# Kernel optimization log

Measured on AMD Instinct MI355X. Metric: run time of the kernel, lower is better.

The kernel has to match this reference:

```python
import jax, jax.numpy as jnp
import numpy as np

# PointPillars KITTI config (matches init_kwargs)
VX, VY = 0.16, 0.16
PC_RANGE = (0.0, -39.68, -3.0, 69.12, 39.68, 1.0)
X_OFFSET = VX / 2 + PC_RANGE[0]          # 0.08
Y_OFFSET = VY / 2 + PC_RANGE[1]          # -39.60
Z_CONST = (PC_RANGE[5] + PC_RANGE[2]) / 2  # -1.0
GRID_X = int((PC_RANGE[3] - PC_RANGE[0]) / VX)  # 432
GRID_Y = int((PC_RANGE[4] - PC_RANGE[1]) / VY)  # 496
BN_EPS = 1e-3


def setup_inputs() -> dict:
    key = jax.random.key(0)
    ks = jax.random.split(key, 6)
    B, PPB, N, C = 4, 12000, 32, 64
    P = B * PPB
    # raw pillar point features (x,y,z,intensity)
    pillars = jax.random.normal(ks[0], (P, N, 4), dtype=jnp.float32)
    # unique pillar cells per batch element (real voxelization never duplicates cells)
    cells = jax.vmap(lambda k: jax.random.permutation(k, GRID_X * GRID_Y)[:PPB])(
        jax.random.split(ks[1], B))  # [B, PPB]
    coors_x = (cells // GRID_Y).reshape(-1).astype(jnp.int64)
    coors_y = (cells % GRID_Y).reshape(-1).astype(jnp.int64)
    coors_b = jnp.repeat(jnp.arange(B, dtype=jnp.int64), PPB)
    npoints = jax.random.randint(ks[2], (P,), 1, N + 1, dtype=jnp.int32)
    W = jax.random.normal(ks[3], (C, 10), dtype=jnp.float32) * 0.1
    gamma = jnp.ones((C,), dtype=jnp.float32)
    beta = jnp.zeros((C,), dtype=jnp.float32)
    return {"pillars": pillars, "W": W, "gamma": gamma, "beta": beta,
            "coors_x": coors_x, "coors_y": coors_y, "coors_b": coors_b,
            "npoints": npoints, "batch_size": B}


def reference(pillars, W, gamma, beta, coors_x, coors_y, coors_b, npoints, batch_size):
    dt = pillars.dtype
    P, N, _ = pillars.shape
    npf = npoints.astype(dt)
    # offset from pillar point-centroid (sum includes zero padding, as in torch)
    mean_xyz = jnp.sum(pillars[:, :, :3], axis=1, keepdims=True) / npf[:, None, None]
    off_center = pillars[:, :, :3] - mean_xyz  # [P,N,3]
    # offset from pillar cell center
    xo = pillars[:, :, 0:1] - (coors_x.astype(dt)[:, None, None] * VX + X_OFFSET)
    yo = pillars[:, :, 1:2] - (coors_y.astype(dt)[:, None, None] * VY + Y_OFFSET)
    zo = jnp.full_like(xo, Z_CONST)
    # features after the in-place overwrite of channels 0,1:
    # [x_off, y_off, z, intensity, dx, dy, dz, x_off, y_off, z_const]
    feats = jnp.concatenate(
        [xo, yo, pillars[:, :, 2:4], off_center, xo, yo, zo], axis=-1)  # [P,N,10]
    mask = (jnp.arange(N)[None, :] < npoints[:, None]).astype(dt)  # [P,N]
    feats = feats * mask[:, :, None]
    # per-point linear (no bias) -> BN (training-mode batch stats over P,N) -> ReLU
    x = jnp.einsum('pnf,cf->pnc', feats, W)  # [P,N,C]
    mu = jnp.mean(x, axis=(0, 1))
    var = jnp.var(x, axis=(0, 1))
    x = (x - mu) * jax.lax.rsqrt(var + BN_EPS) * gamma + beta
    x = jax.nn.relu(x)
    x_max = jnp.max(x, axis=1)  # [P,C] segment-max over points per pillar
    # scatter into dense BEV grid, then [B, C, Y, X]
    C = x_max.shape[-1]
    grid = jnp.zeros((batch_size, GRID_X, GRID_Y, C), dtype=dt)
    grid = grid.at[coors_b, coors_x, coors_y].set(x_max)
    return jnp.transpose(grid, (0, 3, 2, 1))
```

## Files before the change

### kernel.cpp

```cpp
#include <hip/hip_runtime.h>
#include <stdint.h>

#define GRID_X 432
#define GRID_Y 496
#define NB 4
#define NPTS 32
#define NC 64
#define NSLOTS 64
#define CELLS (GRID_Y * GRID_X)

constexpr float VXc = 0.16f, VYc = 0.16f;
constexpr float X_OFFSET = 0.08f, Y_OFFSET = -39.60f, Z_CONST = -1.0f;
constexpr float BN_EPS = 1e-3f;

__global__ __launch_bounds__(256) void pillar_stats_kernel(
    const float* __restrict__ pillars, const float* __restrict__ W,
    const int* __restrict__ cx, const int* __restrict__ cy,
    const int* __restrict__ cb, const int* __restrict__ npoints,
    float* __restrict__ vmax, float* __restrict__ vmin, int* __restrict__ map,
    double* __restrict__ dsum, double* __restrict__ dsq, int P)
{
    __shared__ float4 pts[4][NPTS];
    __shared__ float pinfo[4][4];
    __shared__ float ssum[4][NC], ssq[4][NC];

    const int tid = threadIdx.x;
    const int p0 = blockIdx.x * 4;

    if (tid < 128) {
        int pl = tid >> 5, n = tid & 31;
        int p = p0 + pl;
        float4 v = make_float4(0.f, 0.f, 0.f, 0.f);
        if (p < P) v = ((const float4*)pillars)[(size_t)p * NPTS + n];
        pts[pl][n] = v;
        float sx = v.x, sy = v.y, sz = v.z;
        #pragma unroll
        for (int m = 16; m >= 1; m >>= 1) {
            sx += __shfl_xor(sx, m, 32);
            sy += __shfl_xor(sy, m, 32);
            sz += __shfl_xor(sz, m, 32);
        }
        if (n == 0 && p < P) {
            float npf = (float)npoints[p];
            pinfo[pl][0] = sx / npf;
            pinfo[pl][1] = sy / npf;
            pinfo[pl][2] = sz / npf;
            pinfo[pl][3] = npf;
        }
    }
    if (tid >= 128 && tid < 132) {
        int p = p0 + (tid - 128);
        if (p < P) {
            int b = cb[p];
            map[(size_t)b * CELLS + (size_t)cy[p] * GRID_X + cx[p]] = p;
        }
    }
    __syncthreads();

    const int pl = tid >> 6, c = tid & 63;
    const int p = p0 + pl;
    float ssu = 0.f, sq2 = 0.f;
    if (p < P) {
        const float* w = W + c * 10;
        float w0 = w[0], w1 = w[1], w2 = w[2], w3 = w[3], w4 = w[4];
        float w5 = w[5], w6 = w[6], w7 = w[7], w8 = w[8], w9 = w[9];
        float Aw = w0 + w4 + w7;
        float Bw = w1 + w5 + w8;
        float Cw = w2 + w6;
        float Dw = w3;
        float cxo = cx[p] * VXc + X_OFFSET;
        float cyo = cy[p] * VYc + Y_OFFSET;
        float mx = pinfo[pl][0], my = pinfo[pl][1], mz = pinfo[pl][2];
        int np = (int)pinfo[pl][3];
        float E = -cxo * (w0 + w7) - cyo * (w1 + w8)
                  - mx * w4 - my * w5 - mz * w6 + Z_CONST * w9;
        float smax = -1e30f, smin = 1e30f;
        #pragma unroll
        for (int n = 0; n < NPTS; ++n) {
            float4 pt = pts[pl][n];
            float v = E;
            v = fmaf(pt.x, Aw, v);
            v = fmaf(pt.y, Bw, v);
            v = fmaf(pt.z, Cw, v);
            v = fmaf(pt.w, Dw, v);
            v = (n < np) ? v : 0.0f;
            smax = fmaxf(smax, v);
            smin = fminf(smin, v);
            ssu += v;
            sq2 = fmaf(v, v, sq2);
        }
        vmax[(size_t)p * NC + c] = smax;
        vmin[(size_t)p * NC + c] = smin;
    }
    ssum[pl][c] = ssu;
    ssq[pl][c]  = sq2;
    __syncthreads();
    if (tid < NC) {
        float s = ssum[0][tid] + ssum[1][tid] + ssum[2][tid] + ssum[3][tid];
        float q = ssq[0][tid]  + ssq[1][tid]  + ssq[2][tid]  + ssq[3][tid];
        int slot = blockIdx.x & (NSLOTS - 1);
        atomicAdd(&dsum[slot * NC + tid], (double)s);
        atomicAdd(&dsq[slot * NC + tid],  (double)q);
    }
}

__global__ void bn_params_kernel(const double* __restrict__ dsum,
                                 const double* __restrict__ dsq,
                                 const float* __restrict__ gamma,
                                 const float* __restrict__ beta,
                                 float* __restrict__ st, int P)
{
    int c = threadIdx.x;
    if (c < NC) {
        double s = 0.0, q = 0.0;
        for (int i = 0; i < NSLOTS; ++i) { s += dsum[i * NC + c]; q += dsq[i * NC + c]; }
        double cnt = (double)P * NPTS;
        double mu = s / cnt;
        double var = q / cnt - mu * mu;
        float scale = gamma[c] * (float)(1.0 / sqrt(var + (double)BN_EPS));
        float shift = beta[c] - (float)mu * scale;
        st[c] = scale;
        st[NC + c] = shift;
    }
}

__global__ __launch_bounds__(256) void scatter_out_kernel(
    const int* __restrict__ map, const float* __restrict__ vmax,
    const float* __restrict__ vmin, const float* __restrict__ st,
    float* __restrict__ out)
{
    const int q = blockIdx.x * 256 + threadIdx.x;
    const int b = blockIdx.y;
    const int m = map[(size_t)b * CELLS + q];
    float* ob = out + (size_t)b * NC * CELLS + q;
    #pragma unroll 8
    for (int c = 0; c < NC; ++c) {
        float r = 0.0f;
        if (m >= 0) {
            float s = st[c], t = st[NC + c];
            float v = (s >= 0.0f) ? vmax[(size_t)m * NC + c] : vmin[(size_t)m * NC + c];
            r = fmaxf(fmaf(s, v, t), 0.0f);
        }
        ob[(size_t)c * CELLS] = r;
    }
}

extern "C" void kernel_launch(void* const* d_in, const int* in_sizes, int n_in,
                              void* d_out, int out_size, void* d_ws, size_t ws_size,
                              hipStream_t stream) {
    const float* pillars = (const float*)d_in[0];
    const float* W       = (const float*)d_in[1];
    const float* gamma   = (const float*)d_in[2];
    const float* beta    = (const float*)d_in[3];
    const int*   cx      = (const int*)d_in[4];
    const int*   cy      = (const int*)d_in[5];
    const int*   cb      = (const int*)d_in[6];
    const int*   np      = (const int*)d_in[7];
    const int P = in_sizes[4];

    char* ws = (char*)d_ws;
    float* vmax = (float*)ws;
    float* vmin = vmax + (size_t)P * NC;
    int*   map  = (int*)(vmin + (size_t)P * NC);
    size_t mapN = (size_t)NB * CELLS;
    double* dsum = (double*)(((uintptr_t)(map + mapN) + 255) & ~(uintptr_t)255);
    double* dsq  = dsum + NSLOTS * NC;
    float*  st   = (float*)(dsq + NSLOTS * NC);

    hipMemsetAsync(map, 0xFF, mapN * sizeof(int), stream);
    hipMemsetAsync(dsum, 0, (size_t)NSLOTS * NC * 2 * sizeof(double), stream);

    pillar_stats_kernel<<<(P + 3) / 4, 256, 0, stream>>>(
        pillars, W, cx, cy, cb, np, vmax, vmin, map, dsum, dsq, P);
    bn_params_kernel<<<1, 64, 0, stream>>>(dsum, dsq, gamma, beta, st, P);
    scatter_out_kernel<<<dim3(CELLS / 256, NB), 256, 0, stream>>>(
        map, vmax, vmin, st, (float*)d_out);
}
```

Measured before the change: 287.2 us.

## Fold gamma sign into features to drop vmin; vectorize scatter with float4 stores

Each channel's projected values are multiplied by the sign of gamma, and scale now uses |gamma|. This makes a single max buffer enough for the BN-ReLU-max reduction, so the vmin array and its reads and writes go away. The scatter kernel now handles four grid cells per thread: it loads the map as int4, keeps scale and shift in shared memory, and writes float4 outputs. This is meant to cut store transactions on the large dense output. The cost is four gathered vsel reads per thread per channel.

```diff
diff --git a/kernel.cpp b/kernel.cpp
--- a/kernel.cpp
+++ b/kernel.cpp
@@ -8,6 +8,7 @@
 #define NC 64
 #define NSLOTS 64
 #define CELLS (GRID_Y * GRID_X)
+#define QUADS (CELLS / 4)
 
 constexpr float VXc = 0.16f, VYc = 0.16f;
 constexpr float X_OFFSET = 0.08f, Y_OFFSET = -39.60f, Z_CONST = -1.0f;
@@ -15,13 +16,14 @@
 
 __global__ __launch_bounds__(256) void pillar_stats_kernel(
     const float* __restrict__ pillars, const float* __restrict__ W,
+    const float* __restrict__ gamma,
     const int* __restrict__ cx, const int* __restrict__ cy,
     const int* __restrict__ cb, const int* __restrict__ npoints,
-    float* __restrict__ vmax, float* __restrict__ vmin, int* __restrict__ map,
+    float* __restrict__ vsel, int* __restrict__ map,
     double* __restrict__ dsum, double* __restrict__ dsq, int P)
 {
     __shared__ float4 pts[4][NPTS];
-    __shared__ float pinfo[4][4];
+    __shared__ float pinfo[4][6];
     __shared__ float ssum[4][NC], ssq[4][NC];
 
     const int tid = threadIdx.x;
@@ -46,6 +48,8 @@
             pinfo[pl][1] = sy / npf;
             pinfo[pl][2] = sz / npf;
             pinfo[pl][3] = npf;
+            pinfo[pl][4] = cx[p] * VXc + X_OFFSET;
+            pinfo[pl][5] = cy[p] * VYc + Y_OFFSET;
         }
     }
     if (tid >= 128 && tid < 132) {
@@ -64,17 +68,18 @@
         const float* w = W + c * 10;
         float w0 = w[0], w1 = w[1], w2 = w[2], w3 = w[3], w4 = w[4];
         float w5 = w[5], w6 = w[6], w7 = w[7], w8 = w[8], w9 = w[9];
-        float Aw = w0 + w4 + w7;
-        float Bw = w1 + w5 + w8;
-        float Cw = w2 + w6;
-        float Dw = w3;
-        float cxo = cx[p] * VXc + X_OFFSET;
-        float cyo = cy[p] * VYc + Y_OFFSET;
+        float sg = (gamma[c] >= 0.0f) ? 1.0f : -1.0f;
+        float Aw = sg * (w0 + w4 + w7);
+        float Bw = sg * (w1 + w5 + w8);
+        float Cw = sg * (w2 + w6);
+        float Dw = sg * w3;
+        float cxo = pinfo[pl][4];
+        float cyo = pinfo[pl][5];
         float mx = pinfo[pl][0], my = pinfo[pl][1], mz = pinfo[pl][2];
         int np = (int)pinfo[pl][3];
-        float E = -cxo * (w0 + w7) - cyo * (w1 + w8)
-                  - mx * w4 - my * w5 - mz * w6 + Z_CONST * w9;
-        float smax = -1e30f, smin = 1e30f;
+        float E = sg * (-cxo * (w0 + w7) - cyo * (w1 + w8)
+                        - mx * w4 - my * w5 - mz * w6 + Z_CONST * w9);
+        float smax = -1e30f;
         #pragma unroll
         for (int n = 0; n < NPTS; ++n) {
             float4 pt = pts[pl][n];
@@ -85,12 +90,10 @@
             v = fmaf(pt.w, Dw, v);
             v = (n < np) ? v : 0.0f;
             smax = fmaxf(smax, v);
-            smin = fminf(smin, v);
             ssu += v;
             sq2 = fmaf(v, v, sq2);
         }
-        vmax[(size_t)p * NC + c] = smax;
-        vmin[(size_t)p * NC + c] = smin;
+        vsel[(size_t)p * NC + c] = smax;
     }
     ssum[pl][c] = ssu;
     ssq[pl][c]  = sq2;
@@ -117,7 +120,7 @@
         double cnt = (double)P * NPTS;
         double mu = s / cnt;
         double var = q / cnt - mu * mu;
-        float scale = gamma[c] * (float)(1.0 / sqrt(var + (double)BN_EPS));
+        float scale = fabsf(gamma[c]) * (float)(1.0 / sqrt(var + (double)BN_EPS));
         float shift = beta[c] - (float)mu * scale;
         st[c] = scale;
         st[NC + c] = shift;
@@ -125,23 +128,34 @@
 }
 
 __global__ __launch_bounds__(256) void scatter_out_kernel(
-    const int* __restrict__ map, const float* __restrict__ vmax,
-    const float* __restrict__ vmin, const float* __restrict__ st,
-    float* __restrict__ out)
+    const int* __restrict__ map, const float* __restrict__ vsel,
+    const float* __restrict__ st, float* __restrict__ out)
 {
-    const int q = blockIdx.x * 256 + threadIdx.x;
+    __shared__ float ssc[NC], ssh[NC];
+    if (threadIdx.x < NC) {
+        ssc[threadIdx.x] = st[threadIdx.x];
+        ssh[threadIdx.x] = st[NC + threadIdx.x];
+    }
+    __syncthreads();
+    const int q4 = blockIdx.x * 256 + threadIdx.x;
     const int b = blockIdx.y;
-    const int m = map[(size_t)b * CELLS + q];
-    float* ob = out + (size_t)b * NC * CELLS + q;
+    if (q4 >= QUADS) return;
+    const int4 m4 = ((const int4*)(map + (size_t)b * CELLS))[q4];
+    const bool bx = m4.x >= 0, by = m4.y >= 0, bz = m4.z >= 0, bw = m4.w >= 0;
+    const float* vpx = vsel + (size_t)(bx ? m4.x : 0) * NC;
+    const float* vpy = vsel + (size_t)(by ? m4.y : 0) * NC;
+    const float* vpz = vsel + (size_t)(bz ? m4.z : 0) * NC;
+    const float* vpw = vsel + (size_t)(bw ? m4.w : 0) * NC;
+    float* ob = out + (size_t)b * NC * CELLS + (size_t)q4 * 4;
     #pragma unroll 8
     for (int c = 0; c < NC; ++c) {
-        float r = 0.0f;
-        if (m >= 0) {
-            float s = st[c], t = st[NC + c];
-            float v = (s >= 0.0f) ? vmax[(size_t)m * NC + c] : vmin[(size_t)m * NC + c];
-            r = fmaxf(fmaf(s, v, t), 0.0f);
-        }
-        ob[(size_t)c * CELLS] = r;
+        float sc = ssc[c], sh = ssh[c];
+        float4 r;
+        r.x = bx ? fmaxf(fmaf(sc, vpx[c], sh), 0.0f) : 0.0f;
+        r.y = by ? fmaxf(fmaf(sc, vpy[c], sh), 0.0f) : 0.0f;
+        r.z = bz ? fmaxf(fmaf(sc, vpz[c], sh), 0.0f) : 0.0f;
+        r.w = bw ? fmaxf(fmaf(sc, vpw[c], sh), 0.0f) : 0.0f;
+        *(float4*)(ob + (size_t)c * CELLS) = r;
     }
 }
 
@@ -159,9 +173,8 @@
     const int P = in_sizes[4];
 
     char* ws = (char*)d_ws;
-    float* vmax = (float*)ws;
-    float* vmin = vmax + (size_t)P * NC;
-    int*   map  = (int*)(vmin + (size_t)P * NC);
+    float* vsel = (float*)ws;
+    int*   map  = (int*)(vsel + (size_t)P * NC);
     size_t mapN = (size_t)NB * CELLS;
     double* dsum = (double*)(((uintptr_t)(map + mapN) + 255) & ~(uintptr_t)255);
     double* dsq  = dsum + NSLOTS * NC;
@@ -171,8 +184,8 @@
     hipMemsetAsync(dsum, 0, (size_t)NSLOTS * NC * 2 * sizeof(double), stream);
 
     pillar_stats_kernel<<<(P + 3) / 4, 256, 0, stream>>>(
-        pillars, W, cx, cy, cb, np, vmax, vmin, map, dsum, dsq, P);
+        pillars, W, gamma, cx, cy, cb, np, vsel, map, dsum, dsq, P);
     bn_params_kernel<<<1, 64, 0, stream>>>(dsum, dsq, gamma, beta, st, P);
-    scatter_out_kernel<<<dim3(CELLS / 256, NB), 256, 0, stream>>>(
-        map, vmax, vmin, st, (float*)d_out);
+    scatter_out_kernel<<<dim3((QUADS + 255) / 256, NB), 256, 0, stream>>>(
+        map, vsel, st, (float*)d_out);
 }
```

New measurement: 285.1 us. No clear change (-0.7%).
